# Kernel tuning notes

Hardware: AMD Instinct MI355X
Metric: run time of the kernel (lower is better)

The kernel has to match this reference:

```python
import jax, jax.numpy as jnp
import numpy as np

N_NODES = 40000
N_EDGES = 400000
N_GRAPHS = 64
CONV_DIM = 64
N_FEAT = 9
EDGE_DIM = 3
Z_DIM = 2 * CONV_DIM + EDGE_DIM  # 131


def setup_inputs() -> dict:
    key = jax.random.key(0)
    ks = jax.random.split(key, 32)
    def lin(k, fan_in, fan_out):
        b = 1.0 / np.sqrt(fan_in)
        kw, kb = jax.random.split(k)
        return (jax.random.uniform(kw, (fan_in, fan_out), jnp.float32, -b, b),
                jax.random.uniform(kb, (fan_out,), jnp.float32, -b, b))
    inp = {}
    inp['x'] = jax.random.normal(ks[0], (N_NODES, N_FEAT), jnp.float32)
    inp['edge_index_1'] = jax.random.randint(ks[1], (2, N_EDGES), 0, N_NODES, jnp.int32)
    inp['edge_index_2'] = jax.random.randint(ks[2], (2, N_EDGES), 0, N_NODES, jnp.int32)
    inp['weight_1'] = jax.random.normal(ks[3], (N_EDGES, EDGE_DIM), jnp.float32)
    inp['weight_2'] = jax.random.normal(ks[4], (N_EDGES, EDGE_DIM), jnp.float32)
    # sorted graph ids: 64 graphs of 625 nodes each
    inp['batch'] = jnp.repeat(jnp.arange(N_GRAPHS, dtype=jnp.int32), N_NODES // N_GRAPHS)
    # parameters (stored [in, out])
    inp['fc1_w'], inp['fc1_b'] = lin(ks[5], N_FEAT, CONV_DIM)
    inp['lin_f_w'], inp['lin_f_b'] = lin(ks[6], Z_DIM, CONV_DIM)
    inp['lin_s_w'], inp['lin_s_b'] = lin(ks[7], Z_DIM, CONV_DIM)
    inp['gru_w_ih'], inp['gru_b_ih'] = lin(ks[8], CONV_DIM, 3 * CONV_DIM)  # gate order r,z,n
    inp['gru_w_hh'], inp['gru_b_hh'] = lin(ks[9], CONV_DIM, 3 * CONV_DIM)
    inp['fcs_w'], inp['fcs_b'] = lin(ks[10], CONV_DIM, CONV_DIM)
    inp['fc2c_w'], inp['fc2c_b'] = lin(ks[11], CONV_DIM, 64)
    inp['fc3c_w'], inp['fc3c_b'] = lin(ks[12], 64, 2)
    inp['fc2d_w'], inp['fc2d_b'] = lin(ks[13], CONV_DIM, 64)
    inp['fc3d_w'], inp['fc3d_b'] = lin(ks[14], 64, 2)
    return inp


def _cgconv(x, edge_index, edge_attr, wf, bf, ws, bs):
    # CGConv, flow='target_to_source': x_i = x[row], x_j = x[col], aggregate (mean) at row
    row, col = edge_index[0], edge_index[1]
    z = jnp.concatenate([x[row], x[col], edge_attr], axis=-1)       # [E, 131]
    msg = jax.nn.sigmoid(z @ wf + bf) * jax.nn.softplus(z @ ws + bs)  # [E, C]
    agg = jax.ops.segment_sum(msg, row, num_segments=x.shape[0])
    cnt = jax.ops.segment_sum(jnp.ones((msg.shape[0],), msg.dtype), row, num_segments=x.shape[0])
    return x + agg / jnp.maximum(cnt, 1.0)[:, None]                  # residual


def _gru_step(xt, h, w_ih, w_hh, b_ih, b_hh):
    gi = xt @ w_ih + b_ih
    gh = h @ w_hh + b_hh
    ir, iz, inn = jnp.split(gi, 3, axis=-1)
    hr, hz, hn = jnp.split(gh, 3, axis=-1)
    r = jax.nn.sigmoid(ir + hr)
    zg = jax.nn.sigmoid(iz + hz)
    n = jnp.tanh(inn + r * hn)
    return (1.0 - zg) * n + zg * h


def reference(x, edge_index_1, edge_index_2, weight_1, weight_2, batch,
              fc1_w, fc1_b, lin_f_w, lin_f_b, lin_s_w, lin_s_b,
              gru_w_ih, gru_b_ih, gru_w_hh, gru_b_hh,
              fcs_w, fcs_b, fc2c_w, fc2c_b, fc3c_w, fc3c_b,
              fc2d_w, fc2d_b, fc3d_w, fc3d_b):
    x = jax.nn.relu(x @ fc1_w + fc1_b)          # dropout inactive (eval)
    h = x
    for _ in range(3):                          # 3 GRU refinement iterations
        m = jax.nn.relu(_cgconv(x, edge_index_2, weight_2, lin_f_w, lin_f_b, lin_s_w, lin_s_b))
        m = jax.nn.relu(_cgconv(m, edge_index_1, weight_1, lin_f_w, lin_f_b, lin_s_w, lin_s_b))
        h = _gru_step(m, h, gru_w_ih, gru_w_hh, gru_b_ih, gru_b_hh)
        x = h
    # first node index of each graph (batch is sorted)
    idx_ct = jnp.searchsorted(batch, jnp.arange(N_GRAPHS, dtype=batch.dtype))
    xg = x[idx_ct]                              # [B, C]
    xg = jax.nn.relu(xg @ fcs_w + fcs_b)
    xc = jax.nn.relu(xg @ fc2c_w + fc2c_b)
    x_class = jax.nn.sigmoid(xc @ fc3c_w + fc3c_b)
    xd = jax.nn.relu(xg @ fc2d_w + fc2d_b)
    x_delta = xd @ fc3d_w + fc3d_b
    return (x_class, x_delta)
```

## Files before the change

### kernel.cpp

```cpp
#include <hip/hip_runtime.h>
#include <hip/hip_bf16.h>
#include <hip/hip_fp16.h>
#include <math.h>

constexpr int NE = 400000;
constexpr int NN = 40000;
constexpr int CD = 64;
constexpr int NGRAPH = 64;
constexpr int SCAN_BLOCKS = (NN + 255) / 256;
constexpr int EBLK = (NE + 255) / 256;

typedef _Float16 f16x8 __attribute__((ext_vector_type(8)));
typedef float f32x4 __attribute__((ext_vector_type(4)));

__global__ void k_fc1(const float* __restrict__ x,
                      const float* __restrict__ w,
                      const float* __restrict__ b,
                      float* __restrict__ out) {
    int i = blockIdx.x * 256 + threadIdx.x;
    if (i >= NN * CD) return;
    int n = i >> 6, c = i & 63;
    float acc = b[c];
    #pragma unroll
    for (int k = 0; k < 9; ++k)
        acc = fmaf(x[n * 9 + k], w[k * 64 + c], acc);
    out[i] = fmaxf(acc, 0.f);
}

__global__ void k_count2(const int* __restrict__ ei1, const int* __restrict__ ei2,
                         int* __restrict__ cnt1, int* __restrict__ cnt2) {
    const int b = blockIdx.x;
    const bool s2 = (b >= EBLK);
    const int* ei = s2 ? ei2 : ei1;
    int* cnt = s2 ? cnt2 : cnt1;
    int e = (s2 ? b - EBLK : b) * 256 + threadIdx.x;
    if (e >= NE) return;
    atomicAdd(&cnt[ei[e]], 1);
}

__global__ void k_scan_part2(const int* __restrict__ cnt1, const int* __restrict__ cnt2,
                             int* __restrict__ part1, int* __restrict__ part2) {
    __shared__ int red[256];
    const int b = blockIdx.x;
    const bool s2 = (b >= SCAN_BLOCKS);
    const int* cnt = s2 ? cnt2 : cnt1;
    int* partials = s2 ? part2 : part1;
    const int bb = s2 ? b - SCAN_BLOCKS : b;
    const int tid = threadIdx.x;
    const int i = bb * 256 + tid;
    red[tid] = (i < NN) ? cnt[i] : 0;
    __syncthreads();
    for (int s = 128; s > 0; s >>= 1) {
        if (tid < s) red[tid] += red[tid + s];
        __syncthreads();
    }
    if (tid == 0) partials[bb] = red[0];
}

__global__ void k_scan_mid2(const int* __restrict__ part1, const int* __restrict__ part2,
                            int* __restrict__ offs1, int* __restrict__ offs2) {
    __shared__ int part[256];
    const bool s2 = (blockIdx.x == 1);
    const int* partials = s2 ? part2 : part1;
    int* offs = s2 ? offs2 : offs1;
    const int tid = threadIdx.x;
    const int v = (tid < SCAN_BLOCKS) ? partials[tid] : 0;
    part[tid] = v;
    __syncthreads();
    for (int off = 1; off < 256; off <<= 1) {
        int t = (tid >= off) ? part[tid - off] : 0;
        __syncthreads();
        part[tid] += t;
        __syncthreads();
    }
    if (tid < SCAN_BLOCKS) offs[tid] = part[tid] - v;
}

__global__ void k_scan_fill2(const int* __restrict__ cnt1, const int* __restrict__ cnt2,
                             const int* __restrict__ offs1, const int* __restrict__ offs2,
                             int* __restrict__ rs1, int* __restrict__ rs2,
                             int* __restrict__ cur1, int* __restrict__ cur2) {
    __shared__ int part[256];
    const int b = blockIdx.x;
    const bool s2 = (b >= SCAN_BLOCKS);
    const int* cnt = s2 ? cnt2 : cnt1;
    const int* offs = s2 ? offs2 : offs1;
    int* row_start = s2 ? rs2 : rs1;
    int* cursor = s2 ? cur2 : cur1;
    const int bb = s2 ? b - SCAN_BLOCKS : b;
    const int tid = threadIdx.x;
    const int i = bb * 256 + tid;
    const int v = (i < NN) ? cnt[i] : 0;
    part[tid] = v;
    __syncthreads();
    for (int off = 1; off < 256; off <<= 1) {
        int t = (tid >= off) ? part[tid - off] : 0;
        __syncthreads();
        part[tid] += t;
        __syncthreads();
    }
    const int excl = part[tid] - v + offs[bb];
    if (i < NN) { row_start[i] = excl; cursor[i] = excl; }
    if (i == NN - 1) row_start[NN] = NE;
}

__global__ void k_scatter2(const int* __restrict__ ei1, const int* __restrict__ ei2,
                           int* __restrict__ cur1, int* __restrict__ cur2,
                           int* __restrict__ perm1, int* __restrict__ perm2) {
    const int b = blockIdx.x;
    const bool s2 = (b >= EBLK);
    const int* ei = s2 ? ei2 : ei1;
    int* cursor = s2 ? cur2 : cur1;
    int* perm = s2 ? perm2 : perm1;
    int e = (s2 ? b - EBLK : b) * 256 + threadIdx.x;
    if (e >= NE) return;
    int pos = atomicAdd(&cursor[ei[e]], 1);
    perm[pos] = e;
}

__global__ void k_edge_gather2(const int* __restrict__ ei1, const int* __restrict__ ei2,
                               const float* __restrict__ w1, const float* __restrict__ w2,
                               const int* __restrict__ perm1, const int* __restrict__ perm2,
                               int2* __restrict__ rcP1, int2* __restrict__ rcP2,
                               float4* __restrict__ ewP1, float4* __restrict__ ewP2) {
    const int b = blockIdx.x;
    const bool s2 = (b >= EBLK);
    const int* ei = s2 ? ei2 : ei1;
    const float* ew = s2 ? w2 : w1;
    const int* perm = s2 ? perm2 : perm1;
    int2* rcP = s2 ? rcP2 : rcP1;
    float4* ewP = s2 ? ewP2 : ewP1;
    int p = (s2 ? b - EBLK : b) * 256 + threadIdx.x;
    if (p >= NE) return;
    const int e = perm[p];
    rcP[p] = make_int2(ei[e], ei[NE + e]);
    ewP[p] = make_float4(ew[3 * e], ew[3 * e + 1], ew[3 * e + 2], 0.f);
}

__global__ void k_wt16(const float* __restrict__ lfw, const float* __restrict__ lsw,
                       _Float16* __restrict__ Wt) {
    const int k = blockIdx.x;
    const int c = threadIdx.x;
    float v;
    if (c < 64)       v = lfw[k * 64 + c];
    else if (c < 128) v = lsw[k * 64 + (c - 64)];
    else if (c < 192) v = lfw[(64 + k) * 64 + (c - 128)];
    else              v = lsw[(64 + k) * 64 + (c - 192)];
    Wt[c * 64 + k] = (_Float16)v;
}

__global__ void k_wtg16(const float* __restrict__ wih, const float* __restrict__ whh,
                        _Float16* __restrict__ WtG) {
    const int i = blockIdx.x * 256 + threadIdx.x;
    const int c = i >> 6, k = i & 63;
    const float v = (c < 192) ? wih[k * 192 + c] : whh[k * 192 + (c - 192)];
    WtG[c * 64 + k] = (_Float16)v;
}

__launch_bounds__(256, 4)
__global__ void k_proj_mfma(const float* __restrict__ x,
                            const _Float16* __restrict__ Wt,
                            const float* __restrict__ bfp, const float* __restrict__ bsp,
                            float* __restrict__ Pi, __half2* __restrict__ Pj16) {
    __shared__ _Float16 xs16[32][72];
    const int tid = threadIdx.x;
    const int n0 = blockIdx.x * 32;
    {
        const int n = tid >> 3, k0 = (tid & 7) * 8;
        const float4 a = *(const float4*)&x[(size_t)(n0 + n) * 64 + k0];
        const float4 b = *(const float4*)&x[(size_t)(n0 + n) * 64 + k0 + 4];
        f16x8 v;
        v[0] = (_Float16)a.x; v[1] = (_Float16)a.y; v[2] = (_Float16)a.z; v[3] = (_Float16)a.w;
        v[4] = (_Float16)b.x; v[5] = (_Float16)b.y; v[6] = (_Float16)b.z; v[7] = (_Float16)b.w;
        *(f16x8*)&xs16[n][k0] = v;
    }
    __syncthreads();
    const int l  = tid & 63;
    const int w  = tid >> 6;
    const int lr = l & 15;
    const int kb = l >> 4;
    const int nt = w & 1;
    const f16x8 A0 = *(const f16x8*)&xs16[nt * 16 + lr][kb * 8];
    const f16x8 A1 = *(const f16x8*)&xs16[nt * 16 + lr][32 + kb * 8];
    const int orow = n0 + nt * 16 + kb * 4;

    if (w < 2) {
        for (int ct = 0; ct < 8; ++ct) {
            const int col = ct * 16 + lr;
            const f16x8 B0 = *(const f16x8*)&Wt[col * 64 + kb * 8];
            const f16x8 B1 = *(const f16x8*)&Wt[col * 64 + 32 + kb * 8];
            f32x4 acc = {0.f, 0.f, 0.f, 0.f};
            acc = __builtin_amdgcn_mfma_f32_16x16x32_f16(A0, B0, acc, 0, 0, 0);
            acc = __builtin_amdgcn_mfma_f32_16x16x32_f16(A1, B1, acc, 0, 0, 0);
            const float bias = (col < 64) ? bfp[col] : bsp[col - 64];
            #pragma unroll
            for (int r = 0; r < 4; ++r)
                Pi[(size_t)(orow + r) * 128 + col] = acc[r] + bias;
        }
    } else {
        for (int pt = 0; pt < 4; ++pt) {
            const int colF = 128 + pt * 16 + lr;
            const int colS = 192 + pt * 16 + lr;
            const f16x8 BF0 = *(const f16x8*)&Wt[colF * 64 + kb * 8];
            const f16x8 BF1 = *(const f16x8*)&Wt[colF * 64 + 32 + kb * 8];
            const f16x8 BS0 = *(const f16x8*)&Wt[colS * 64 + kb * 8];
            const f16x8 BS1 = *(const f16x8*)&Wt[colS * 64 + 32 + kb * 8];
            f32x4 aF = {0.f, 0.f, 0.f, 0.f}, aS = {0.f, 0.f, 0.f, 0.f};
            aF = __builtin_amdgcn_mfma_f32_16x16x32_f16(A0, BF0, aF, 0, 0, 0);
            aF = __builtin_amdgcn_mfma_f32_16x16x32_f16(A1, BF1, aF, 0, 0, 0);
            aS = __builtin_amdgcn_mfma_f32_16x16x32_f16(A0, BS0, aS, 0, 0, 0);
            aS = __builtin_amdgcn_mfma_f32_16x16x32_f16(A1, BS1, aS, 0, 0, 0);
            const int cj = pt * 16 + lr;
            #pragma unroll
            for (int r = 0; r < 4; ++r)
                Pj16[(size_t)(orow + r) * 64 + cj] = __floats2half2_rn((float)aF[r], (float)aS[r]);
        }
    }
}

__launch_bounds__(256, 7)
__global__ void k_edge_range(const __half2* __restrict__ Pj,
                             const float* __restrict__ Pi,
                             const int2* __restrict__ rcP, const float4* __restrict__ ewP,
                             const float* __restrict__ wfe, const float* __restrict__ wse,
                             const int* __restrict__ rs,
                             const float* __restrict__ xin, float* __restrict__ out) {
    __shared__ __align__(16) float piS[8][128];
    __shared__ __align__(16) float accS[8][8][64];
    __shared__ int rsS[9];
    const int tid = threadIdx.x;
    const int hw = tid >> 5;
    const int hb = hw & 1;
    const int wv = tid >> 6;
    const int c2 = (tid & 31) * 2;
    const int r0 = blockIdx.x * 8;
    for (int i = tid; i < 1024; i += 256)
        piS[i >> 7][i & 127] = Pi[(size_t)r0 * 128 + i];
    for (int i = tid; i < 4096; i += 256)
        ((float*)accS)[i] = 0.f;
    if (tid < 9) rsS[tid] = rs[r0 + tid];
    __syncthreads();
    const float wf0a = wfe[c2],       wf0b = wfe[c2 + 1];
    const float wf1a = wfe[64 + c2],  wf1b = wfe[64 + c2 + 1];
    const float wf2a = wfe[128 + c2], wf2b = wfe[128 + c2 + 1];
    const float ws0a = wse[c2],       ws0b = wse[c2 + 1];
    const float ws1a = wse[64 + c2],  ws1b = wse[64 + c2 + 1];
    const float ws2a = wse[128 + c2], ws2b = wse[128 + c2 + 1];
    const int pbeg = rsS[0], pend = rsS[8];

#define EDGE_BODY(P)                                                              \
    {                                                                             \
        const int2 rc = rcP[P];                                                   \
        const float4 e = ewP[P];                                                  \
        const uint2 Jraw = *(const uint2*)&Pj[rc.y * 64 + c2];                    \
        const float2 Ja = __half22float2(*(const __half2*)&Jraw.x);               \
        const float2 Jb = __half22float2(*(const __half2*)&Jraw.y);               \
        const int row = rc.x - r0;                                                \
        const float2 pf = *(const float2*)&piS[row][c2];                          \
        const float2 ps = *(const float2*)&piS[row][64 + c2];                     \
        const float afa = pf.x + Ja.x + e.x * wf0a + e.y * wf1a + e.z * wf2a;     \
        const float asa = ps.x + Ja.y + e.x * ws0a + e.y * ws1a + e.z * ws2a;     \
        const float afb = pf.y + Jb.x + e.x * wf0b + e.y * wf1b + e.z * wf2b;     \
        const float asb = ps.y + Jb.y + e.x * ws0b + e.y * ws1b + e.z * ws2b;     \
        const float sga = 1.f / (1.f + __expf(-afa));                             \
        const float spa = (asa > 20.f) ? asa : __logf(1.f + __expf(asa));         \
        const float sgb = 1.f / (1.f + __expf(-afb));                             \
        const float spb = (asb > 20.f) ? asb : __logf(1.f + __expf(asb));         \
        float2 acc = *(const float2*)&accS[hw][row][c2];                          \
        acc.x = fmaf(sga, spa, acc.x);                                            \
        acc.y = fmaf(sgb, spb, acc.y);                                            \
        *(float2*)&accS[hw][row][c2] = acc;                                       \
    }

    int p0 = pbeg + 2 * wv;
    #pragma unroll 2
    for (; p0 + 2 <= pend; p0 += 8) {
        const int p = p0 + hb;
        EDGE_BODY(p)
    }
    {
        const int p = p0 + hb;
        if (p < pend) EDGE_BODY(p)
    }
#undef EDGE_BODY

    __syncthreads();
    for (int i = tid; i < 512; i += 256) {
        const int row = i >> 6, ch = i & 63;
        float s = 0.f;
        #pragma unroll
        for (int a = 0; a < 8; ++a) s += accS[a][row][ch];
        const int deg = rsS[row + 1] - rsS[row];
        const size_t o = (size_t)(r0 + row) * 64 + ch;
        out[o] = fmaxf(fmaf(s, 1.f / (float)max(deg, 1), xin[o]), 0.f);
    }
}

__global__ void k_gru_mfma(const float* __restrict__ m, float* __restrict__ h,
                           const _Float16* __restrict__ WtG,
                           const float* __restrict__ bih, const float* __restrict__ bhh) {
    __shared__ _Float16 ms16[32][72];
    __shared__ _Float16 hs16[32][72];
    __shared__ __align__(16) float hs32[32][64];
    const int tid = threadIdx.x;
    const int n0 = blockIdx.x * 32;
    {
        const int n = tid >> 3, k0 = (tid & 7) * 8;
        const float4 ma = *(const float4*)&m[(size_t)(n0 + n) * 64 + k0];
        const float4 mb = *(const float4*)&m[(size_t)(n0 + n) * 64 + k0 + 4];
        const float4 ha = *(const float4*)&h[(size_t)(n0 + n) * 64 + k0];
        const float4 hb = *(const float4*)&h[(size_t)(n0 + n) * 64 + k0 + 4];
        f16x8 mv, hv;
        mv[0] = (_Float16)ma.x; mv[1] = (_Float16)ma.y; mv[2] = (_Float16)ma.z; mv[3] = (_Float16)ma.w;
        mv[4] = (_Float16)mb.x; mv[5] = (_Float16)mb.y; mv[6] = (_Float16)mb.z; mv[7] = (_Float16)mb.w;
        hv[0] = (_Float16)ha.x; hv[1] = (_Float16)ha.y; hv[2] = (_Float16)ha.z; hv[3] = (_Float16)ha.w;
        hv[4] = (_Float16)hb.x; hv[5] = (_Float16)hb.y; hv[6] = (_Float16)hb.z; hv[7] = (_Float16)hb.w;
        *(f16x8*)&ms16[n][k0] = mv;
        *(f16x8*)&hs16[n][k0] = hv;
        *(float4*)&hs32[n][k0] = ha;
        *(float4*)&hs32[n][k0 + 4] = hb;
    }
    __syncthreads();
    const int l  = tid & 63;
    const int w  = tid >> 6;
    const int lr = l & 15;
    const int kb = l >> 4;
    const int nt = w & 1;
    const int cg = w >> 1;
    const f16x8 A0 = *(const f16x8*)&ms16[nt * 16 + lr][kb * 8];
    const f16x8 A1 = *(const f16x8*)&ms16[nt * 16 + lr][32 + kb * 8];
    const f16x8 H0 = *(const f16x8*)&hs16[nt * 16 + lr][kb * 8];
    const f16x8 H1 = *(const f16x8*)&hs16[nt * 16 + lr][32 + kb * 8];
    const int orow = n0 + nt * 16 + kb * 4;
    const int lrow = nt * 16 + kb * 4;

    #pragma unroll
    for (int t = 0; t < 2; ++t) {
        const int ct = cg + t * 2;
        const int c = ct * 16 + lr;
        const f16x8 BiR0 = *(const f16x8*)&WtG[(c)       * 64 + kb * 8];
        const f16x8 BiR1 = *(const f16x8*)&WtG[(c)       * 64 + 32 + kb * 8];
        const f16x8 BiZ0 = *(const f16x8*)&WtG[(64 + c)  * 64 + kb * 8];
        const f16x8 BiZ1 = *(const f16x8*)&WtG[(64 + c)  * 64 + 32 + kb * 8];
        const f16x8 BiN0 = *(const f16x8*)&WtG[(128 + c) * 64 + kb * 8];
        const f16x8 BiN1 = *(const f16x8*)&WtG[(128 + c) * 64 + 32 + kb * 8];
        const f16x8 BhR0 = *(const f16x8*)&WtG[(192 + c) * 64 + kb * 8];
        const f16x8 BhR1 = *(const f16x8*)&WtG[(192 + c) * 64 + 32 + kb * 8];
        const f16x8 BhZ0 = *(const f16x8*)&WtG[(256 + c) * 64 + kb * 8];
        const f16x8 BhZ1 = *(const f16x8*)&WtG[(256 + c) * 64 + 32 + kb * 8];
        const f16x8 BhN0 = *(const f16x8*)&WtG[(320 + c) * 64 + kb * 8];
        const f16x8 BhN1 = *(const f16x8*)&WtG[(320 + c) * 64 + 32 + kb * 8];
        f32x4 aIR = {0,0,0,0}, aIZ = {0,0,0,0}, aIN = {0,0,0,0};
        f32x4 aHR = {0,0,0,0}, aHZ = {0,0,0,0}, aHN = {0,0,0,0};
        aIR = __builtin_amdgcn_mfma_f32_16x16x32_f16(A0, BiR0, aIR, 0, 0, 0);
        aIR = __builtin_amdgcn_mfma_f32_16x16x32_f16(A1, BiR1, aIR, 0, 0, 0);
        aIZ = __builtin_amdgcn_mfma_f32_16x16x32_f16(A0, BiZ0, aIZ, 0, 0, 0);
        aIZ = __builtin_amdgcn_mfma_f32_16x16x32_f16(A1, BiZ1, aIZ, 0, 0, 0);
        aIN = __builtin_amdgcn_mfma_f32_16x16x32_f16(A0, BiN0, aIN, 0, 0, 0);
        aIN = __builtin_amdgcn_mfma_f32_16x16x32_f16(A1, BiN1, aIN, 0, 0, 0);
        aHR = __builtin_amdgcn_mfma_f32_16x16x32_f16(H0, BhR0, aHR, 0, 0, 0);
        aHR = __builtin_amdgcn_mfma_f32_16x16x32_f16(H1, BhR1, aHR, 0, 0, 0);
        aHZ = __builtin_amdgcn_mfma_f32_16x16x32_f16(H0, BhZ0, aHZ, 0, 0, 0);
        aHZ = __builtin_amdgcn_mfma_f32_16x16x32_f16(H1, BhZ1, aHZ, 0, 0, 0);
        aHN = __builtin_amdgcn_mfma_f32_16x16x32_f16(H0, BhN0, aHN, 0, 0, 0);
        aHN = __builtin_amdgcn_mfma_f32_16x16x32_f16(H1, BhN1, aHN, 0, 0, 0);
        const float bir = bih[c], biz = bih[64 + c], bin = bih[128 + c];
        const float bhr = bhh[c], bhz = bhh[64 + c], bhn = bhh[128 + c];
        #pragma unroll
        for (int r = 0; r < 4; ++r) {
            const float rg = 1.f / (1.f + __expf(-(((float)aIR[r] + bir) + ((float)aHR[r] + bhr))));
            const float zg = 1.f / (1.f + __expf(-(((float)aIZ[r] + biz) + ((float)aHZ[r] + bhz))));
            const float ng = tanhf(((float)aIN[r] + bin) + rg * ((float)aHN[r] + bhn));
            h[(size_t)(orow + r) * 64 + c] = (1.f - zg) * ng + zg * hs32[lrow + r][c];
        }
    }
}

__global__ void k_idx(const int* __restrict__ batch, int* __restrict__ idx) {
    int g = threadIdx.x;
    if (g >= NGRAPH) return;
    int lo = 0, hi = NN;
    while (lo < hi) {
        int mid = (lo + hi) >> 1;
        if (batch[mid] < g) lo = mid + 1; else hi = mid;
    }
    idx[g] = lo;
}

__global__ void k_head(const float* __restrict__ h, const int* __restrict__ idx,
                       const float* __restrict__ fcsw, const float* __restrict__ fcsb,
                       const float* __restrict__ f2cw, const float* __restrict__ f2cb,
                       const float* __restrict__ f3cw, const float* __restrict__ f3cb,
                       const float* __restrict__ f2dw, const float* __restrict__ f2db,
                       const float* __restrict__ f3dw, const float* __restrict__ f3db,
                       float* __restrict__ out) {
    __shared__ float hsB[4096];
    __shared__ float waB[4096];
    __shared__ float wbB[4096];
    __shared__ float wcB[4096];
    const int tid = threadIdx.x;
    for (int i = tid; i < 4096; i += 256) {
        int g = i >> 6, k = i & 63;
        hsB[i] = h[(size_t)idx[g] * 64 + k];
        waB[i] = fcsw[i];
        wbB[i] = f2cw[i];
        wcB[i] = f2dw[i];
    }
    __syncthreads();
    float v[16];
    #pragma unroll
    for (int j = 0; j < 16; ++j) {
        const int i = j * 256 + tid, g = i >> 6, c = i & 63;
        float a = fcsb[c];
        for (int k = 0; k < 64; ++k) a = fmaf(hsB[g * 64 + k], waB[k * 64 + c], a);
        v[j] = fmaxf(a, 0.f);
    }
    __syncthreads();
    #pragma unroll
    for (int j = 0; j < 16; ++j) hsB[j * 256 + tid] = v[j];
    __syncthreads();
    float vc[16], vd[16];
    #pragma unroll
    for (int j = 0; j < 16; ++j) {
        const int i = j * 256 + tid, g = i >> 6, c = i & 63;
        float a1 = f2cb[c], a2 = f2db[c];
        for (int k = 0; k < 64; ++k) {
            const float xv = hsB[g * 64 + k];
            a1 = fmaf(xv, wbB[k * 64 + c], a1);
            a2 = fmaf(xv, wcB[k * 64 + c], a2);
        }
        vc[j] = fmaxf(a1, 0.f);
        vd[j] = fmaxf(a2, 0.f);
    }
    __syncthreads();
    #pragma unroll
    for (int j = 0; j < 16; ++j) {
        waB[j * 256 + tid] = vc[j];
        wbB[j * 256 + tid] = vd[j];
    }
    if (tid < 128) wcB[tid] = f3cw[tid];
    else           wcB[tid] = f3dw[tid - 128];
    __syncthreads();
    if (tid < 128) {
        int g = tid >> 1, j = tid & 1;
        float a = f3cb[j];
        for (int k = 0; k < 64; ++k) a = fmaf(waB[g * 64 + k], wcB[k * 2 + j], a);
        out[g * 2 + j] = 1.f / (1.f + expf(-a));
    } else {
        int t = tid - 128, g = t >> 1, j = t & 1;
        float a = f3db[j];
        for (int k = 0; k < 64; ++k) a = fmaf(wbB[g * 64 + k], wcB[128 + k * 2 + j], a);
        out[128 + g * 2 + j] = a;
    }
}

extern "C" void kernel_launch(void* const* d_in, const int* in_sizes, int n_in,
                              void* d_out, int out_size, void* d_ws, size_t ws_size,
                              hipStream_t stream) {
    (void)in_sizes; (void)n_in; (void)out_size; (void)ws_size;
    const float* x    = (const float*)d_in[0];
    const int* ei1    = (const int*)d_in[1];
    const int* ei2    = (const int*)d_in[2];
    const float* w1   = (const float*)d_in[3];
    const float* w2   = (const float*)d_in[4];
    const int* batch  = (const int*)d_in[5];
    const float* fc1w = (const float*)d_in[6];
    const float* fc1b = (const float*)d_in[7];
    const float* lfw  = (const float*)d_in[8];
    const float* lfb  = (const float*)d_in[9];
    const float* lsw  = (const float*)d_in[10];
    const float* lsb  = (const float*)d_in[11];
    const float* wih  = (const float*)d_in[12];
    const float* bih  = (const float*)d_in[13];
    const float* whh  = (const float*)d_in[14];
    const float* bhh  = (const float*)d_in[15];
    const float* fcsw = (const float*)d_in[16];
    const float* fcsb = (const float*)d_in[17];
    const float* f2cw = (const float*)d_in[18];
    const float* f2cb = (const float*)d_in[19];
    const float* f3cw = (const float*)d_in[20];
    const float* f3cb = (const float*)d_in[21];
    const float* f2dw = (const float*)d_in[22];
    const float* f2db = (const float*)d_in[23];
    const float* f3dw = (const float*)d_in[24];
    const float* f3db = (const float*)d_in[25];

    char* ws = (char*)d_ws;
    size_t off = 0;
    auto alloc = [&](size_t bytes) { char* p = ws + off; off += (bytes + 255) & ~size_t(255); return p; };
    float*   Pi    = (float*)alloc(size_t(NN) * 128 * 4);
    __half2* Pj16  = (__half2*)alloc(size_t(NN) * 64 * 4);
    float*   hbuf  = (float*)alloc(size_t(NN) * CD * 4);
    float*   mbuf  = (float*)alloc(size_t(NN) * CD * 4);
    _Float16* W16  = (_Float16*)alloc(256 * 64 * 2);
    _Float16* WG16 = (_Float16*)alloc(384 * 64 * 2);
    int*   cnt1  = (int*)alloc(size_t(NN) * 4);
    int*   cnt2  = (int*)alloc(size_t(NN) * 4);
    int*   rs1   = (int*)alloc(size_t(NN + 1) * 4);
    int*   rs2   = (int*)alloc(size_t(NN + 1) * 4);
    int*   cur1  = (int*)alloc(size_t(NN + 1) * 4);
    int*   cur2  = (int*)alloc(size_t(NN + 1) * 4);
    int*   perm1 = (int*)alloc(size_t(NE) * 4);
    int*   perm2 = (int*)alloc(size_t(NE) * 4);
    int2*  rcP1  = (int2*)alloc(size_t(NE) * 8);
    int2*  rcP2  = (int2*)alloc(size_t(NE) * 8);
    float4* ewP1 = (float4*)alloc(size_t(NE) * 16);
    float4* ewP2 = (float4*)alloc(size_t(NE) * 16);
    int*   part1 = (int*)alloc(256 * 4);
    int*   part2 = (int*)alloc(256 * 4);
    int*   offs1 = (int*)alloc(256 * 4);
    int*   offs2 = (int*)alloc(256 * 4);
    int*   idx   = (int*)alloc(256);

    const int NB_NC = (NN * CD + 255) / 256;
    const int EDGE_BLOCKS = NN / 8;
    const int PROJ_BLOCKS = NN / 32;
    const int GRU_BLOCKS  = NN / 32;

    const float* lfe = lfw + 128 * 64;
    const float* lse = lsw + 128 * 64;

    hipMemsetAsync(cnt1, 0, size_t(NN) * 4 * 2 + 256, stream);
    k_count2<<<2 * EBLK, 256, 0, stream>>>(ei1, ei2, cnt1, cnt2);
    k_scan_part2<<<2 * SCAN_BLOCKS, 256, 0, stream>>>(cnt1, cnt2, part1, part2);
    k_scan_mid2<<<2, 256, 0, stream>>>(part1, part2, offs1, offs2);
    k_scan_fill2<<<2 * SCAN_BLOCKS, 256, 0, stream>>>(cnt1, cnt2, offs1, offs2, rs1, rs2, cur1, cur2);
    k_scatter2<<<2 * EBLK, 256, 0, stream>>>(ei1, ei2, cur1, cur2, perm1, perm2);
    k_edge_gather2<<<2 * EBLK, 256, 0, stream>>>(ei1, ei2, w1, w2, perm1, perm2,
                                                 rcP1, rcP2, ewP1, ewP2);
    k_wt16<<<64, 256, 0, stream>>>(lfw, lsw, W16);
    k_wtg16<<<96, 256, 0, stream>>>(wih, whh, WG16);

    k_fc1<<<NB_NC, 256, 0, stream>>>(x, fc1w, fc1b, hbuf);

    for (int it = 0; it < 3; ++it) {
        k_proj_mfma<<<PROJ_BLOCKS, 256, 0, stream>>>(hbuf, W16, lfb, lsb, Pi, Pj16);
        k_edge_range<<<EDGE_BLOCKS, 256, 0, stream>>>(Pj16, Pi, rcP2, ewP2,
                                                      lfe, lse, rs2, hbuf, mbuf);
        k_proj_mfma<<<PROJ_BLOCKS, 256, 0, stream>>>(mbuf, W16, lfb, lsb, Pi, Pj16);
        k_edge_range<<<EDGE_BLOCKS, 256, 0, stream>>>(Pj16, Pi, rcP1, ewP1,
                                                      lfe, lse, rs1, mbuf, mbuf);
        k_gru_mfma<<<GRU_BLOCKS, 256, 0, stream>>>(mbuf, hbuf, WG16, bih, bhh);
    }

    k_idx<<<1, 64, 0, stream>>>(batch, idx);
    k_head<<<1, 256, 0, stream>>>(hbuf, idx, fcsw, fcsb, f2cw, f2cb, f3cw, f3cb,
                                  f2dw, f2db, f3dw, f3db, (float*)d_out);
}
```

Baseline: 590.6 us.

## Fuse scatter with gather, fold idx into head, store Pi as half in LDS

Merges the CSR scatter and edge-gather kernels so each edge writes its row/col and weights straight to the slot it claims atomically, which removes the perm buffer and one launch. Folds the graph-index binary search into the head kernel to drop another launch. In the edge kernel the per-row Pi projections are packed into half2 in shared memory, cutting LDS use, and launch bounds go from 7 to 8 blocks per CU for more occupancy. The half-precision Pi adds rounding error, and edge order within a row is now nondeterministic, as it was before.

```diff
diff --git a/kernel.cpp b/kernel.cpp
--- a/kernel.cpp
+++ b/kernel.cpp
@@ -104,37 +104,25 @@
     if (i == NN - 1) row_start[NN] = NE;
 }
 
-__global__ void k_scatter2(const int* __restrict__ ei1, const int* __restrict__ ei2,
-                           int* __restrict__ cur1, int* __restrict__ cur2,
-                           int* __restrict__ perm1, int* __restrict__ perm2) {
-    const int b = blockIdx.x;
-    const bool s2 = (b >= EBLK);
-    const int* ei = s2 ? ei2 : ei1;
-    int* cursor = s2 ? cur2 : cur1;
-    int* perm = s2 ? perm2 : perm1;
-    int e = (s2 ? b - EBLK : b) * 256 + threadIdx.x;
-    if (e >= NE) return;
-    int pos = atomicAdd(&cursor[ei[e]], 1);
-    perm[pos] = e;
-}
-
-__global__ void k_edge_gather2(const int* __restrict__ ei1, const int* __restrict__ ei2,
-                               const float* __restrict__ w1, const float* __restrict__ w2,
-                               const int* __restrict__ perm1, const int* __restrict__ perm2,
-                               int2* __restrict__ rcP1, int2* __restrict__ rcP2,
-                               float4* __restrict__ ewP1, float4* __restrict__ ewP2) {
+__global__ void k_scatgath2(const int* __restrict__ ei1, const int* __restrict__ ei2,
+                            const float* __restrict__ w1, const float* __restrict__ w2,
+                            int* __restrict__ cur1, int* __restrict__ cur2,
+                            int2* __restrict__ rcP1, int2* __restrict__ rcP2,
+                            float4* __restrict__ ewP1, float4* __restrict__ ewP2) {
     const int b = blockIdx.x;
     const bool s2 = (b >= EBLK);
     const int* ei = s2 ? ei2 : ei1;
     const float* ew = s2 ? w2 : w1;
-    const int* perm = s2 ? perm2 : perm1;
+    int* cursor = s2 ? cur2 : cur1;
     int2* rcP = s2 ? rcP2 : rcP1;
     float4* ewP = s2 ? ewP2 : ewP1;
-    int p = (s2 ? b - EBLK : b) * 256 + threadIdx.x;
-    if (p >= NE) return;
-    const int e = perm[p];
-    rcP[p] = make_int2(ei[e], ei[NE + e]);
-    ewP[p] = make_float4(ew[3 * e], ew[3 * e + 1], ew[3 * e + 2], 0.f);
+    int e = (s2 ? b - EBLK : b) * 256 + threadIdx.x;
+    if (e >= NE) return;
+    const int r = ei[e];
+    const int c = ei[NE + e];
+    const int pos = atomicAdd(&cursor[r], 1);
+    rcP[pos] = make_int2(r, c);
+    ewP[pos] = make_float4(ew[3 * e], ew[3 * e + 1], ew[3 * e + 2], 0.f);
 }
 
 __global__ void k_wt16(const float* __restrict__ lfw, const float* __restrict__ lsw,
@@ -218,14 +206,14 @@
     }
 }
 
-__launch_bounds__(256, 7)
+__launch_bounds__(256, 8)
 __global__ void k_edge_range(const __half2* __restrict__ Pj,
                              const float* __restrict__ Pi,
                              const int2* __restrict__ rcP, const float4* __restrict__ ewP,
                              const float* __restrict__ wfe, const float* __restrict__ wse,
                              const int* __restrict__ rs,
                              const float* __restrict__ xin, float* __restrict__ out) {
-    __shared__ __align__(16) float piS[8][128];
+    __shared__ __align__(8) __half2 piH[8][64];
     __shared__ __align__(16) float accS[8][8][64];
     __shared__ int rsS[9];
     const int tid = threadIdx.x;
@@ -234,8 +222,11 @@
     const int wv = tid >> 6;
     const int c2 = (tid & 31) * 2;
     const int r0 = blockIdx.x * 8;
-    for (int i = tid; i < 1024; i += 256)
-        piS[i >> 7][i & 127] = Pi[(size_t)r0 * 128 + i];
+    for (int i = tid; i < 512; i += 256) {
+        const int row = i >> 6, ch = i & 63;
+        piH[row][ch] = __floats2half2_rn(Pi[(size_t)(r0 + row) * 128 + ch],
+                                         Pi[(size_t)(r0 + row) * 128 + 64 + ch]);
+    }
     for (int i = tid; i < 4096; i += 256)
         ((float*)accS)[i] = 0.f;
     if (tid < 9) rsS[tid] = rs[r0 + tid];
@@ -256,12 +247,13 @@
         const float2 Ja = __half22float2(*(const __half2*)&Jraw.x);               \
         const float2 Jb = __half22float2(*(const __half2*)&Jraw.y);               \
         const int row = rc.x - r0;                                                \
-        const float2 pf = *(const float2*)&piS[row][c2];                          \
-        const float2 ps = *(const float2*)&piS[row][64 + c2];                     \
-        const float afa = pf.x + Ja.x + e.x * wf0a + e.y * wf1a + e.z * wf2a;     \
-        const float asa = ps.x + Ja.y + e.x * ws0a + e.y * ws1a + e.z * ws2a;     \
-        const float afb = pf.y + Jb.x + e.x * wf0b + e.y * wf1b + e.z * wf2b;     \
-        const float asb = ps.y + Jb.y + e.x * ws0b + e.y * ws1b + e.z * ws2b;     \
+        const uint2 PH = *(const uint2*)&piH[row][c2];                            \
+        const float2 Pa = __half22float2(*(const __half2*)&PH.x);                 \
+        const float2 Pb = __half22float2(*(const __half2*)&PH.y);                 \
+        const float afa = Pa.x + Ja.x + e.x * wf0a + e.y * wf1a + e.z * wf2a;     \
+        const float asa = Pa.y + Ja.y + e.x * ws0a + e.y * ws1a + e.z * ws2a;     \
+        const float afb = Pb.x + Jb.x + e.x * wf0b + e.y * wf1b + e.z * wf2b;     \
+        const float asb = Pb.y + Jb.y + e.x * ws0b + e.y * ws1b + e.z * ws2b;     \
         const float sga = 1.f / (1.f + __expf(-afa));                             \
         const float spa = (asa > 20.f) ? asa : __logf(1.f + __expf(asa));         \
         const float sgb = 1.f / (1.f + __expf(-afb));                             \
@@ -376,18 +368,7 @@
     }
 }
 
-__global__ void k_idx(const int* __restrict__ batch, int* __restrict__ idx) {
-    int g = threadIdx.x;
-    if (g >= NGRAPH) return;
-    int lo = 0, hi = NN;
-    while (lo < hi) {
-        int mid = (lo + hi) >> 1;
-        if (batch[mid] < g) lo = mid + 1; else hi = mid;
-    }
-    idx[g] = lo;
-}
-
-__global__ void k_head(const float* __restrict__ h, const int* __restrict__ idx,
+__global__ void k_head(const float* __restrict__ h, const int* __restrict__ batch,
                        const float* __restrict__ fcsw, const float* __restrict__ fcsb,
                        const float* __restrict__ f2cw, const float* __restrict__ f2cb,
                        const float* __restrict__ f3cw, const float* __restrict__ f3cb,
@@ -398,10 +379,20 @@
     __shared__ float waB[4096];
     __shared__ float wbB[4096];
     __shared__ float wcB[4096];
-    const int tid = threadIdx.x;
+    __shared__ int sidx[64];
+    const int tid = threadIdx.x;
+    if (tid < 64) {
+        int lo = 0, hi = NN;
+        while (lo < hi) {
+            int mid = (lo + hi) >> 1;
+            if (batch[mid] < tid) lo = mid + 1; else hi = mid;
+        }
+        sidx[tid] = lo;
+    }
+    __syncthreads();
     for (int i = tid; i < 4096; i += 256) {
         int g = i >> 6, k = i & 63;
-        hsB[i] = h[(size_t)idx[g] * 64 + k];
+        hsB[i] = h[(size_t)sidx[g] * 64 + k];
         waB[i] = fcsw[i];
         wbB[i] = f2cw[i];
         wcB[i] = f2dw[i];
@@ -500,8 +491,6 @@
     int*   rs2   = (int*)alloc(size_t(NN + 1) * 4);
     int*   cur1  = (int*)alloc(size_t(NN + 1) * 4);
     int*   cur2  = (int*)alloc(size_t(NN + 1) * 4);
-    int*   perm1 = (int*)alloc(size_t(NE) * 4);
-    int*   perm2 = (int*)alloc(size_t(NE) * 4);
     int2*  rcP1  = (int2*)alloc(size_t(NE) * 8);
     int2*  rcP2  = (int2*)alloc(size_t(NE) * 8);
     float4* ewP1 = (float4*)alloc(size_t(NE) * 16);
@@ -510,7 +499,6 @@
     int*   part2 = (int*)alloc(256 * 4);
     int*   offs1 = (int*)alloc(256 * 4);
     int*   offs2 = (int*)alloc(256 * 4);
-    int*   idx   = (int*)alloc(256);
 
     const int NB_NC = (NN * CD + 255) / 256;
     const int EDGE_BLOCKS = NN / 8;
@@ -525,9 +513,8 @@
     k_scan_part2<<<2 * SCAN_BLOCKS, 256, 0, stream>>>(cnt1, cnt2, part1, part2);
     k_scan_mid2<<<2, 256, 0, stream>>>(part1, part2, offs1, offs2);
     k_scan_fill2<<<2 * SCAN_BLOCKS, 256, 0, stream>>>(cnt1, cnt2, offs1, offs2, rs1, rs2, cur1, cur2);
-    k_scatter2<<<2 * EBLK, 256, 0, stream>>>(ei1, ei2, cur1, cur2, perm1, perm2);
-    k_edge_gather2<<<2 * EBLK, 256, 0, stream>>>(ei1, ei2, w1, w2, perm1, perm2,
-                                                 rcP1, rcP2, ewP1, ewP2);
+    k_scatgath2<<<2 * EBLK, 256, 0, stream>>>(ei1, ei2, w1, w2, cur1, cur2,
+                                              rcP1, rcP2, ewP1, ewP2);
     k_wt16<<<64, 256, 0, stream>>>(lfw, lsw, W16);
     k_wtg16<<<96, 256, 0, stream>>>(wih, whh, WG16);
 
@@ -543,7 +530,6 @@
         k_gru_mfma<<<GRU_BLOCKS, 256, 0, stream>>>(mbuf, hbuf, WG16, bih, bhh);
     }
 
-    k_idx<<<1, 64, 0, stream>>>(batch, idx);
-    k_head<<<1, 256, 0, stream>>>(hbuf, idx, fcsw, fcsb, f2cw, f2cb, f3cw, f3cb,
+    k_head<<<1, 256, 0, stream>>>(hbuf, batch, fcsw, fcsb, f2cw, f2cb, f3cw, f3cb,
                                   f2dw, f2db, f3dw, f3db, (float*)d_out);
 }
```

Result: faster. 563.2 us (-4.6%).
